# Performance work log

Measured on AMD Instinct MI355X. Metric: run time of the kernel, lower is better.

Reference implementation:

```python
import jax, jax.numpy as jnp
import numpy as np

EMB_DIM = 128
WALK_LEN = 40
WINDOW = 5
NEG_SIZE = 5
NEG_WEIGHT = 1.0
NUM_NODES = 1_000_000
BATCH = 512


def _pair_indices(walk_length=WALK_LEN, window_size=WINDOW):
    # replicates the idx_list_src / idx_list_dst construction in __init__
    src, dst = [], []
    for i in range(walk_length):
        for j in range(max(0, i - window_size), i):
            src.append(j); dst.append(i)
        for j in range(i + 1, min(walk_length, i + 1 + window_size)):
            src.append(j); dst.append(i)
    return np.asarray(src, dtype=np.int64), np.asarray(dst, dtype=np.int64)

_SRC, _DST = _pair_indices()  # each has 370 entries
NUM_PAIRS = _SRC.shape[0]


def setup_inputs() -> dict:
    key = jax.random.key(0)
    k1, k2, k3, k4 = jax.random.split(key, 4)
    batch_walk = jax.random.randint(k1, (BATCH, WALK_LEN), 0, NUM_NODES, dtype=jnp.int64)
    neg_idx_dst = jax.random.randint(k2, (BATCH * NUM_PAIRS * NEG_SIZE,), 0, BATCH * WALK_LEN, dtype=jnp.int64)
    init_range = 1.0 / EMB_DIM
    node_embed = jax.random.normal(k3, (NUM_NODES, EMB_DIM), dtype=jnp.float32) * init_range
    context_embed = jax.random.normal(k4, (NUM_NODES, EMB_DIM), dtype=jnp.float32) * init_range
    return {"batch_walk": batch_walk, "neg_idx_dst": neg_idx_dst,
            "node_embed": node_embed, "context_embed": context_embed}


def reference(batch_walk, neg_idx_dst, node_embed, context_embed):
    B = batch_walk.shape[0]
    flat_walk = batch_walk.reshape(-1)                      # [B*L]
    batch_node = node_embed[flat_walk]                      # [B*L, D]
    batch_ctx = context_embed[flat_walk]                    # [B*L, D]

    offsets = (jnp.arange(B, dtype=jnp.int64) * WALK_LEN)[:, None]
    idx_src = (offsets + jnp.asarray(_SRC)[None, :]).reshape(-1)  # [B*370]
    idx_dst = (offsets + jnp.asarray(_DST)[None, :]).reshape(-1)  # [B*370]

    pos_src = batch_node[idx_src]
    pos_dst = batch_ctx[idx_dst]
    pos_score = jnp.clip(jnp.sum(pos_src * pos_dst, axis=1), -6.0, 6.0)
    pos_loss = jnp.mean(-jax.nn.log_sigmoid(pos_score))

    neg_idx_src = jnp.repeat(idx_dst, NEG_SIZE)             # [B*370*NEG]
    neg_src = batch_node[neg_idx_src]
    neg_dst = batch_ctx[neg_idx_dst]
    neg_score = jnp.clip(jnp.sum(neg_src * neg_dst, axis=1), -6.0, 6.0)
    neg_loss = jnp.mean(-jax.nn.log_sigmoid(-neg_score)) * NEG_SIZE * NEG_WEIGHT

    return pos_loss + neg_loss
```

## Files before the change

### kernel.cpp

```cpp
#include <hip/hip_runtime.h>

#define WALK_LEN 40
#define WINDOW   5
#define NPAIRS   370
#define BATCHSZ  512
#define NEGK     5
#define NPOS     (BATCHSZ * NPAIRS)
#define EMB      128
#define NQ       (BATCHSZ * WALK_LEN)
#define THREADS  512
#define GROUPS   (THREADS / 8)
#define HALFP    185
#define NBLOCKS  (BATCHSZ * 2)

struct PairTab { short src[NPAIRS]; short dst[NPAIRS]; };

constexpr PairTab make_pairs() {
    PairTab t{};
    int k = 0;
    for (int i = 0; i < WALK_LEN; ++i) {
        int lo = (i - WINDOW > 0) ? (i - WINDOW) : 0;
        for (int j = lo; j < i; ++j) { t.src[k] = (short)j; t.dst[k] = (short)i; ++k; }
        int hi = (i + 1 + WINDOW < WALK_LEN) ? (i + 1 + WINDOW) : WALK_LEN;
        for (int j = i + 1; j < hi; ++j) { t.src[k] = (short)j; t.dst[k] = (short)i; ++k; }
    }
    return t;
}

__constant__ PairTab g_pairs = make_pairs();

__device__ __forceinline__ unsigned short bf16rn(float f) {
    unsigned u = __float_as_uint(f);
    u += 0x7fffu + ((u >> 16) & 1u);
    return (unsigned short)(u >> 16);
}

__device__ __forceinline__ float softplus_fast(float x) {
    return __logf(1.0f + __expf(x));
}

template <int CTRL>
__device__ __forceinline__ float dpp_add(float x) {
    int y = __builtin_amdgcn_update_dpp(0, __float_as_int(x), CTRL, 0xF, 0xF, true);
    return x + __int_as_float(y);
}
__device__ __forceinline__ float grp8_sum(float d) {
    d = dpp_add<0xB1>(d);
    d = dpp_add<0x4E>(d);
    d = dpp_add<0x141>(d);
    return d;
}

#define UNPACK_U4(u, f, base)                                         \
    do {                                                              \
        _Pragma("unroll")                                             \
        for (int _i = 0; _i < 4; ++_i) {                              \
            const unsigned _v = (&(u).x)[_i];                         \
            (f)[(base) + 2 * _i]     = __uint_as_float(_v << 16);     \
            (f)[(base) + 2 * _i + 1] = __uint_as_float(_v & 0xffff0000u); \
        }                                                             \
    } while (0)

__device__ __forceinline__ float dot_pk(const float* nf, uint4 xa, uint4 xb) {
    float s0 = 0.f, s1 = 0.f, s2 = 0.f, s3 = 0.f;
    #pragma unroll
    for (int i = 0; i < 4; ++i) {
        const unsigned v = (&xa.x)[i];
        s0 = fmaf(__uint_as_float(v << 16),          nf[2 * i],     s0);
        s1 = fmaf(__uint_as_float(v & 0xffff0000u),  nf[2 * i + 1], s1);
    }
    #pragma unroll
    for (int i = 0; i < 4; ++i) {
        const unsigned v = (&xb.x)[i];
        s2 = fmaf(__uint_as_float(v << 16),          nf[8 + 2 * i],     s2);
        s3 = fmaf(__uint_as_float(v & 0xffff0000u),  nf[8 + 2 * i + 1], s3);
    }
    return (s0 + s1) + (s2 + s3);
}

__global__ __launch_bounds__(256) void dw_gather(
    const int*   __restrict__ walk,
    const float* __restrict__ nodeE,
    const float* __restrict__ ctxE,
    unsigned short* __restrict__ dN,
    unsigned short* __restrict__ dC,
    float* __restrict__ out)
{
    if (blockIdx.x == 0 && threadIdx.x == 0) out[0] = 0.f;
    int idx = blockIdx.x * 256 + threadIdx.x;
    const int is_ctx = (idx >= NQ * 32);
    if (is_ctx) idx -= NQ * 32;
    const int q = idx >> 5, c = idx & 31;
    const int row = walk[q];
    const float* src = (is_ctx ? ctxE : nodeE) + (size_t)row * EMB;
    const float4 v = *((const float4*)src + c);
    ushort4 o;
    o.x = bf16rn(v.x); o.y = bf16rn(v.y); o.z = bf16rn(v.z); o.w = bf16rn(v.w);
    unsigned short* dst = (is_ctx ? dC : dN) + (size_t)q * EMB;
    *((ushort4*)dst + c) = o;
}

#define SLOT_DECL(S)                                                        \
    const int  jj##S = (S) * GROUPS + grp;                                  \
    const int  j##S  = jbase + ((jj##S < HALFP) ? jj##S : 0);               \
    const int* nb##S = negdst + ((size_t)b * NPAIRS + j##S) * NEGK;         \
    const int  qa##S = nb##S[0], qb##S = nb##S[1], qc##S = nb##S[2],        \
               qd##S = nb##S[3], qe##S = nb##S[4];                          \
    const uint4* ga##S = (const uint4*)(dC + (size_t)qa##S * EMB);          \
    const uint4* gb##S = (const uint4*)(dC + (size_t)qb##S * EMB);          \
    const uint4* gc##S = (const uint4*)(dC + (size_t)qc##S * EMB);          \
    const uint4* gd##S = (const uint4*)(dC + (size_t)qd##S * EMB);          \
    const uint4* ge##S = (const uint4*)(dC + (size_t)qe##S * EMB);          \
    const uint4 xa0##S = ga##S[lane8], xa1##S = ga##S[lane8 + 8];           \
    const uint4 xb0##S = gb##S[lane8], xb1##S = gb##S[lane8 + 8];           \
    const uint4 xc0##S = gc##S[lane8], xc1##S = gc##S[lane8 + 8];           \
    const uint4 xd0##S = gd##S[lane8], xd1##S = gd##S[lane8 + 8];           \
    const uint4 xe0##S = ge##S[lane8], xe1##S = ge##S[lane8 + 8];

#define SLOT_COMPUTE(S)                                                     \
    if (jj##S < HALFP) {                                                    \
        const int sj = g_pairs.src[j##S];                                   \
        const int dj = g_pairs.dst[j##S];                                   \
        const uint4* rN = (const uint4*)(sN + sj * 64);                     \
        const uint4* rC = (const uint4*)(sC + dj * 64);                     \
        const uint4* rS = (const uint4*)(sN + dj * 64);                     \
        const uint4 a0 = rN[lane8], a1 = rN[lane8 + 8];                     \
        const uint4 c0 = rC[lane8], c1 = rC[lane8 + 8];                     \
        const uint4 n0 = rS[lane8], n1 = rS[lane8 + 8];                     \
        float af[16];                                                       \
        UNPACK_U4(a0, af, 0); UNPACK_U4(a1, af, 8);                         \
        const float dp = grp8_sum(dot_pk(af, c0, c1));                      \
        float nf[16];                                                       \
        UNPACK_U4(n0, nf, 0); UNPACK_U4(n1, nf, 8);                         \
        const float d0 = grp8_sum(dot_pk(nf, xa0##S, xa1##S));              \
        const float d1 = grp8_sum(dot_pk(nf, xb0##S, xb1##S));              \
        const float d2 = grp8_sum(dot_pk(nf, xc0##S, xc1##S));              \
        const float d3 = grp8_sum(dot_pk(nf, xd0##S, xd1##S));              \
        const float d4 = grp8_sum(dot_pk(nf, xe0##S, xe1##S));              \
        acc += softplus_fast(-fminf(6.f, fmaxf(-6.f, dp)));                 \
        acc += softplus_fast( fminf(6.f, fmaxf(-6.f, d0)));                 \
        acc += softplus_fast( fminf(6.f, fmaxf(-6.f, d1)));                 \
        acc += softplus_fast( fminf(6.f, fmaxf(-6.f, d2)));                 \
        acc += softplus_fast( fminf(6.f, fmaxf(-6.f, d3)));                 \
        acc += softplus_fast( fminf(6.f, fmaxf(-6.f, d4)));                 \
    }

__global__ __launch_bounds__(THREADS, 2) void dw_score(
    const int* __restrict__ negdst,
    const unsigned short* __restrict__ dN,
    const unsigned short* __restrict__ dC,
    float* __restrict__ out)
{
    __shared__ unsigned int sN[WALK_LEN * 64];
    __shared__ unsigned int sC[WALK_LEN * 64];
    __shared__ float wsum[THREADS / 64];

    const int b    = blockIdx.x >> 1;
    const int half = blockIdx.x & 1;
    const int tid  = threadIdx.x;

    {
        const uint4* srcN = (const uint4*)(dN + (size_t)b * WALK_LEN * EMB);
        const uint4* srcC = (const uint4*)(dC + (size_t)b * WALK_LEN * EMB);
        for (int u = tid; u < WALK_LEN * 16; u += THREADS) {
            ((uint4*)sN)[u] = srcN[u];
            ((uint4*)sC)[u] = srcC[u];
        }
    }
    __syncthreads();

    const int lane8 = tid & 7;
    const int grp   = tid >> 3;
    const int jbase = half * HALFP;
    float acc = 0.0f;

    SLOT_DECL(0)
    SLOT_DECL(1)
    SLOT_DECL(2)
    SLOT_COMPUTE(0)
    SLOT_COMPUTE(1)
    SLOT_COMPUTE(2)

    acc += __shfl_xor(acc, 8);
    acc += __shfl_xor(acc, 16);
    acc += __shfl_xor(acc, 32);

    if ((tid & 63) == 0) wsum[tid >> 6] = acc;
    __syncthreads();
    if (tid == 0) {
        float tot = 0.f;
        #pragma unroll
        for (int w = 0; w < THREADS / 64; ++w) tot += wsum[w];
        atomicAdd(out, tot * (1.0f / (float)NPOS));
    }
}

extern "C" void kernel_launch(void* const* d_in, const int* in_sizes, int n_in,
                              void* d_out, int out_size, void* d_ws, size_t ws_size,
                              hipStream_t stream) {
    const int*   walk   = (const int*)d_in[0];
    const int*   negdst = (const int*)d_in[1];
    const float* nodeE  = (const float*)d_in[2];
    const float* ctxE   = (const float*)d_in[3];
    float*       out    = (float*)d_out;

    unsigned short* dN = (unsigned short*)d_ws;
    unsigned short* dC = dN + (size_t)NQ * EMB;

    dw_gather<<<(2 * NQ * 32) / 256, 256, 0, stream>>>(walk, nodeE, ctxE, dN, dC, out);
    dw_score<<<NBLOCKS, THREADS, 0, stream>>>(negdst, dN, dC, out);
}
```

Baseline: 39.73 us.

## Switch staging to fp16 with packed half2 dot products and merged log

The staged embedding rows are now converted to fp16 instead of bf16, and each dot product is computed with packed __hfma2 half2 FMAs. This removes the per-element unpacking to fp32. The six softplus terms per pair are combined by multiplying their (1+exp) factors and taking a single log, which saves five log calls. The risks are fp16 accumulation error over 16 products per lane and lower precision from the merged log, though the product of six factors is bounded by about (1+e^6)^6 and fits in fp32.

```diff
diff --git a/kernel.cpp b/kernel.cpp
--- a/kernel.cpp
+++ b/kernel.cpp
@@ -1,4 +1,5 @@
 #include <hip/hip_runtime.h>
+#include <hip/hip_fp16.h>
 
 #define WALK_LEN 40
 #define WINDOW   5
@@ -29,16 +30,6 @@
 
 __constant__ PairTab g_pairs = make_pairs();
 
-__device__ __forceinline__ unsigned short bf16rn(float f) {
-    unsigned u = __float_as_uint(f);
-    u += 0x7fffu + ((u >> 16) & 1u);
-    return (unsigned short)(u >> 16);
-}
-
-__device__ __forceinline__ float softplus_fast(float x) {
-    return __logf(1.0f + __expf(x));
-}
-
 template <int CTRL>
 __device__ __forceinline__ float dpp_add(float x) {
     int y = __builtin_amdgcn_update_dpp(0, __float_as_int(x), CTRL, 0xF, 0xF, true);
@@ -51,31 +42,24 @@
     return d;
 }
 
-#define UNPACK_U4(u, f, base)                                         \
-    do {                                                              \
-        _Pragma("unroll")                                             \
-        for (int _i = 0; _i < 4; ++_i) {                              \
-            const unsigned _v = (&(u).x)[_i];                         \
-            (f)[(base) + 2 * _i]     = __uint_as_float(_v << 16);     \
-            (f)[(base) + 2 * _i + 1] = __uint_as_float(_v & 0xffff0000u); \
-        }                                                             \
-    } while (0)
-
-__device__ __forceinline__ float dot_pk(const float* nf, uint4 xa, uint4 xb) {
-    float s0 = 0.f, s1 = 0.f, s2 = 0.f, s3 = 0.f;
+__device__ __forceinline__ float h2dot(uint4 A0, uint4 A1, uint4 C0, uint4 C1) {
+    const __half2* a0 = (const __half2*)&A0;
+    const __half2* a1 = (const __half2*)&A1;
+    const __half2* c0 = (const __half2*)&C0;
+    const __half2* c1 = (const __half2*)&C1;
+    __half2 h0 = __float2half2_rn(0.f);
+    __half2 h1 = __float2half2_rn(0.f);
     #pragma unroll
     for (int i = 0; i < 4; ++i) {
-        const unsigned v = (&xa.x)[i];
-        s0 = fmaf(__uint_as_float(v << 16),          nf[2 * i],     s0);
-        s1 = fmaf(__uint_as_float(v & 0xffff0000u),  nf[2 * i + 1], s1);
+        h0 = __hfma2(a0[i], c0[i], h0);
+        h1 = __hfma2(a1[i], c1[i], h1);
     }
-    #pragma unroll
-    for (int i = 0; i < 4; ++i) {
-        const unsigned v = (&xb.x)[i];
-        s2 = fmaf(__uint_as_float(v << 16),          nf[8 + 2 * i],     s2);
-        s3 = fmaf(__uint_as_float(v & 0xffff0000u),  nf[8 + 2 * i + 1], s3);
-    }
-    return (s0 + s1) + (s2 + s3);
+    const __half2 hs = __hadd2(h0, h1);
+    return __low2float(hs) + __high2float(hs);
+}
+
+__device__ __forceinline__ float clip6(float x) {
+    return fminf(6.f, fmaxf(-6.f, x));
 }
 
 __global__ __launch_bounds__(256) void dw_gather(
@@ -95,7 +79,10 @@
     const float* src = (is_ctx ? ctxE : nodeE) + (size_t)row * EMB;
     const float4 v = *((const float4*)src + c);
     ushort4 o;
-    o.x = bf16rn(v.x); o.y = bf16rn(v.y); o.z = bf16rn(v.z); o.w = bf16rn(v.w);
+    o.x = __half_as_ushort(__float2half(v.x));
+    o.y = __half_as_ushort(__float2half(v.y));
+    o.z = __half_as_ushort(__float2half(v.z));
+    o.w = __half_as_ushort(__float2half(v.w));
     unsigned short* dst = (is_ctx ? dC : dN) + (size_t)q * EMB;
     *((ushort4*)dst + c) = o;
 }
@@ -127,22 +114,17 @@
         const uint4 a0 = rN[lane8], a1 = rN[lane8 + 8];                     \
         const uint4 c0 = rC[lane8], c1 = rC[lane8 + 8];                     \
         const uint4 n0 = rS[lane8], n1 = rS[lane8 + 8];                     \
-        float af[16];                                                       \
-        UNPACK_U4(a0, af, 0); UNPACK_U4(a1, af, 8);                         \
-        const float dp = grp8_sum(dot_pk(af, c0, c1));                      \
-        float nf[16];                                                       \
-        UNPACK_U4(n0, nf, 0); UNPACK_U4(n1, nf, 8);                         \
-        const float d0 = grp8_sum(dot_pk(nf, xa0##S, xa1##S));              \
-        const float d1 = grp8_sum(dot_pk(nf, xb0##S, xb1##S));              \
-        const float d2 = grp8_sum(dot_pk(nf, xc0##S, xc1##S));              \
-        const float d3 = grp8_sum(dot_pk(nf, xd0##S, xd1##S));              \
-        const float d4 = grp8_sum(dot_pk(nf, xe0##S, xe1##S));              \
-        acc += softplus_fast(-fminf(6.f, fmaxf(-6.f, dp)));                 \
-        acc += softplus_fast( fminf(6.f, fmaxf(-6.f, d0)));                 \
-        acc += softplus_fast( fminf(6.f, fmaxf(-6.f, d1)));                 \
-        acc += softplus_fast( fminf(6.f, fmaxf(-6.f, d2)));                 \
-        acc += softplus_fast( fminf(6.f, fmaxf(-6.f, d3)));                 \
-        acc += softplus_fast( fminf(6.f, fmaxf(-6.f, d4)));                 \
+        const float sp = clip6(grp8_sum(h2dot(a0, a1, c0, c1)));            \
+        const float s0 = clip6(grp8_sum(h2dot(n0, n1, xa0##S, xa1##S)));    \
+        const float s1 = clip6(grp8_sum(h2dot(n0, n1, xb0##S, xb1##S)));    \
+        const float s2 = clip6(grp8_sum(h2dot(n0, n1, xc0##S, xc1##S)));    \
+        const float s3 = clip6(grp8_sum(h2dot(n0, n1, xd0##S, xd1##S)));    \
+        const float s4 = clip6(grp8_sum(h2dot(n0, n1, xe0##S, xe1##S)));    \
+        \
+        const float p0 = (1.f + __expf(-sp)) * (1.f + __expf(s0));          \
+        const float p1 = (1.f + __expf(s1))  * (1.f + __expf(s2));          \
+        const float p2 = (1.f + __expf(s3))  * (1.f + __expf(s4));          \
+        acc += __logf(p0 * p1 * p2);                                        \
     }
 
 __global__ __launch_bounds__(THREADS, 2) void dw_score(
```

After: 38.15 us. 1.04x faster.
